# Optimization experiments

Measured on AMD Instinct MI355X. Metric: run time of the kernel, lower is better.

## Reference

```python
import jax, jax.numpy as jnp
import numpy as np

N_NODES = 500000


def _gconv(x, src, dst, ew, w_neigh, b, w_self):
    # DGL GraphConv(norm='none'): multiply weight first (in>=out here), then aggregate.
    h = x @ w_neigh                      # [N, out]
    msg = h[src] * ew[:, None]           # [E, out]
    agg = jax.ops.segment_sum(msg, dst, num_segments=N_NODES)
    return agg + b + x @ w_self          # neigh conv (+bias) + self-loop linear (no bias)


def setup_inputs() -> dict:
    key = jax.random.key(0)
    ks = jax.random.split(key, 16)
    N, E, G, F = N_NODES, 16000000, 64, 16
    inp = {
        "x": jax.random.normal(ks[0], (N, F), jnp.float32),
        "src": jax.random.randint(ks[1], (E,), 0, N),
        "dst": jax.random.randint(ks[2], (E,), 0, N),
        "graph_id": jnp.sort(jax.random.randint(ks[3], (N,), 0, G)),
        "edge_weight": jax.random.uniform(ks[4], (E,), jnp.float32),
        "num_graphs": G,
        "w_neigh0": jax.random.normal(ks[5], (F, 1), jnp.float32),
        "b0": jax.random.normal(ks[6], (1,), jnp.float32),
        "w_self0": jax.random.normal(ks[7], (F, 1), jnp.float32),
        "w_neigh1": jax.random.normal(ks[8], (1, 1), jnp.float32),
        "b1": jax.random.normal(ks[9], (1,), jnp.float32),
        "w_self1": jax.random.normal(ks[10], (1, 1), jnp.float32),
        "w_neigh2": jax.random.normal(ks[11], (1, 1), jnp.float32),
        "b2": jax.random.normal(ks[12], (1,), jnp.float32),
        "w_self2": jax.random.normal(ks[13], (1, 1), jnp.float32),
        "fc1_w": jax.random.normal(ks[14], (8, 1), jnp.float32),
        "fc1_b": jax.random.normal(ks[15], (8,), jnp.float32),
        "out_w": jax.random.normal(jax.random.fold_in(key, 100), (4, 8), jnp.float32),
        "out_b": jax.random.normal(jax.random.fold_in(key, 101), (4,), jnp.float32),
    }
    return inp


def reference(x, src, dst, graph_id, edge_weight, num_graphs,
              w_neigh0, b0, w_self0, w_neigh1, b1, w_self1,
              w_neigh2, b2, w_self2, fc1_w, fc1_b, out_w, out_b):
    h = jax.nn.relu(_gconv(x, src, dst, edge_weight, w_neigh0, b0, w_self0))
    h = jax.nn.relu(_gconv(h, src, dst, edge_weight, w_neigh1, b1, w_self1))
    h = jax.nn.relu(_gconv(h, src, dst, edge_weight, w_neigh2, b2, w_self2))
    # dgl.sum_nodes: per-graph segment sum over batched graph -> [G, 1]
    hg = jax.ops.segment_sum(h, graph_id, num_segments=num_graphs)
    hg2 = jax.nn.sigmoid((hg @ fc1_w.T + fc1_b) * 1000.0)   # [G, 8]
    out = jax.nn.relu(hg2 @ out_w.T + out_b)                # [G, 4]
    return jax.nn.log_softmax(out, axis=1)
```

## Files before the change

### kernel.cpp

```cpp
#include <hip/hip_runtime.h>

#define N_NODES   500000
#define NGRAPH    64
#define FDIM      16
#define NPB       4096
#define NPB_SHIFT 12
#define NBINS     123
#define NBLK      1024
#define CH        4096
typedef unsigned int u32;
typedef unsigned long long u64;

__global__ __launch_bounds__(1024) void proj_hist(const int* __restrict__ dst, int E, int chunk,
                                                  u32* __restrict__ blockHist,
                                                  const float* __restrict__ x,
                                                  const float* __restrict__ wn,
                                                  const float* __restrict__ wsf,
                                                  float* __restrict__ a,
                                                  float* __restrict__ s) {
    __shared__ u32 cnt[NBINS];
    if (blockIdx.x < NBLK) {
        for (int t = threadIdx.x; t < NBINS; t += 1024) cnt[t] = 0;
        __syncthreads();
        int b = blockIdx.x;
        int lo = b * chunk, hi = min(lo + chunk, E);
        int m = (hi - lo) & ~3;
        for (int i = lo + threadIdx.x * 4; i < lo + m; i += 4096) {
            int4 d = *(const int4*)(dst + i);
            atomicAdd(&cnt[((u32)d.x) >> NPB_SHIFT], 1u);
            atomicAdd(&cnt[((u32)d.y) >> NPB_SHIFT], 1u);
            atomicAdd(&cnt[((u32)d.z) >> NPB_SHIFT], 1u);
            atomicAdd(&cnt[((u32)d.w) >> NPB_SHIFT], 1u);
        }
        for (int i = lo + m + threadIdx.x; i < hi; i += 1024)
            atomicAdd(&cnt[((u32)dst[i]) >> NPB_SHIFT], 1u);
        __syncthreads();
        for (int t = threadIdx.x; t < NBINS; t += 1024)
            blockHist[(size_t)b * NBINS + t] = cnt[t];
    } else {
        int i = (blockIdx.x - NBLK) * 1024 + threadIdx.x;
        if (i >= N_NODES) return;
        const float4* xr = (const float4*)(x + (size_t)i * FDIM);
        float4 v0 = xr[0], v1 = xr[1], v2 = xr[2], v3 = xr[3];
        const float4* n4 = (const float4*)wn;
        const float4* s4 = (const float4*)wsf;
        float4 n0 = n4[0], n1 = n4[1], n2 = n4[2], n3 = n4[3];
        float4 w0 = s4[0], w1 = s4[1], w2 = s4[2], w3 = s4[3];
        float an = v0.x*n0.x + v0.y*n0.y + v0.z*n0.z + v0.w*n0.w
                 + v1.x*n1.x + v1.y*n1.y + v1.z*n1.z + v1.w*n1.w
                 + v2.x*n2.x + v2.y*n2.y + v2.z*n2.z + v2.w*n2.w
                 + v3.x*n3.x + v3.y*n3.y + v3.z*n3.z + v3.w*n3.w;
        float as = v0.x*w0.x + v0.y*w0.y + v0.z*w0.z + v0.w*w0.w
                 + v1.x*w1.x + v1.y*w1.y + v1.z*w1.z + v1.w*w1.w
                 + v2.x*w2.x + v2.y*w2.y + v2.z*w2.z + v2.w*w2.w
                 + v3.x*w3.x + v3.y*w3.y + v3.z*w3.z + v3.w*w3.w;
        a[i] = an;
        s[i] = as;
    }
}

__global__ __launch_bounds__(NBLK) void scan1_kernel(u32* __restrict__ blockHist,
                                                     u32* __restrict__ binTotal) {
    int j = blockIdx.x;
    __shared__ u32 lsum[NBLK];
    int t = threadIdx.x;
    u32 v = blockHist[(size_t)t * NBINS + j];
    lsum[t] = v;
    __syncthreads();
    u32 x = v;
    for (int off = 1; off < NBLK; off <<= 1) {
        u32 y = (t >= off) ? lsum[t - off] : 0u;
        __syncthreads();
        x += y; lsum[t] = x;
        __syncthreads();
    }
    if (t == NBLK - 1) binTotal[j] = x;
    blockHist[(size_t)t * NBINS + j] = x - v;
}

__global__ void scan2_kernel(const u32* __restrict__ binTotal, u32* __restrict__ binStart) {
    __shared__ u32 sh[128];
    int t = threadIdx.x;
    u32 v = (t < NBINS) ? binTotal[t] : 0u;
    sh[t] = v;
    __syncthreads();
    for (int d = 1; d < 128; d <<= 1) {
        u32 y = (t >= d) ? sh[t - d] : 0u;
        __syncthreads();
        sh[t] += y;
        __syncthreads();
    }
    if (t < NBINS) binStart[t] = sh[t] - v;
    if (t == 127) binStart[NBINS] = sh[127];
}

__global__ __launch_bounds__(512) void scatter_staged(const int* __restrict__ src,
                                                      const int* __restrict__ dst,
                                                      const float* __restrict__ ew,
                                                      int E, int chunk,
                                                      const u32* __restrict__ blockHist,
                                                      const u32* __restrict__ binStart,
                                                      u64* __restrict__ binned) {
    __shared__ u32 cursor[NBINS];
    __shared__ u32 cnt[NBINS];
    __shared__ u32 off[NBINS];
    __shared__ u64 stage[CH];
    __shared__ unsigned char binOf[CH];
    int b   = blockIdx.x;
    int tid = threadIdx.x;
    for (int t = tid; t < NBINS; t += 512)
        cursor[t] = binStart[t] + blockHist[(size_t)b * NBINS + t];
    int lo = b * chunk, hiB = min(lo + chunk, E);
    for (int base = lo; base < hiB; base += CH) {
        int n = min(CH, hiB - base);
        for (int t = tid; t < NBINS; t += 512) cnt[t] = 0;
        __syncthreads();
        u32 rec[8]; float wv[8]; u32 bi[8]; u32 rk[8];
#pragma unroll
        for (int k = 0; k < 8; ++k) {
            int idx = base + k * 512 + tid;
            bi[k] = 0xFFFFFFFFu;
            if (idx < base + n) {
                u32 d  = (u32)dst[idx];
                bi[k]  = d >> NPB_SHIFT;
                rec[k] = ((u32)src[idx]) | ((d & (NPB - 1)) << 19);
                wv[k]  = ew[idx];
                rk[k]  = atomicAdd(&cnt[bi[k]], 1u);
            }
        }
        __syncthreads();
        if (tid < NBINS) off[tid] = cnt[tid];
        __syncthreads();
        for (int d2 = 1; d2 < 128; d2 <<= 1) {
            u32 v = 0;
            if (tid < NBINS) { v = off[tid]; if (tid >= d2) v += off[tid - d2]; }
            __syncthreads();
            if (tid < NBINS) off[tid] = v;
            __syncthreads();
        }
        if (tid < NBINS) off[tid] -= cnt[tid];
        __syncthreads();
#pragma unroll
        for (int k = 0; k < 8; ++k) {
            if (bi[k] != 0xFFFFFFFFu) {
                u32 p = off[bi[k]] + rk[k];
                stage[p] = (u64)rec[k] | ((u64)__float_as_uint(wv[k]) << 32);
                binOf[p] = (unsigned char)bi[k];
            }
        }
        __syncthreads();
        for (int p = tid; p < n; p += 512) {
            u32 j = binOf[p];
            binned[cursor[j] + ((u32)p - off[j])] = stage[p];
        }
        __syncthreads();
        for (int t = tid; t < NBINS; t += 512) cursor[t] += cnt[t];
        __syncthreads();
    }
}

template<int S>
__global__ __launch_bounds__(512) void bin_pass(const u64* __restrict__ binned,
                                                const u32* __restrict__ binStart,
                                                const float* __restrict__ hsrc,
                                                float* __restrict__ partials) {
    __shared__ float acc[NPB];
    int blk   = blockIdx.x;
    int j     = blk / S;
    int slice = blk % S;
    for (int t = threadIdx.x; t < NPB; t += 512) acc[t] = 0.0f;
    __syncthreads();
    u32 blo = binStart[j], bhi = binStart[j + 1];
    u32 cnt = bhi - blo;
    u32 per = (cnt + S - 1) / S;
    u32 lo = blo + slice * per;
    u32 hi = min(lo + per, bhi);

    u32 i = lo + threadIdx.x;
    for (; i + 7u * 512u < hi; i += 8u * 512u) {
        u64 e[8];
#pragma unroll
        for (int k = 0; k < 8; ++k) e[k] = __builtin_nontemporal_load(&binned[i + (u32)k * 512u]);
        float g[8];
#pragma unroll
        for (int k = 0; k < 8; ++k) g[k] = hsrc[((u32)e[k]) & 0x7FFFFu];
#pragma unroll
        for (int k = 0; k < 8; ++k)
            atomicAdd(&acc[((u32)e[k]) >> 19], g[k] * __uint_as_float((u32)(e[k] >> 32)));
    }
    for (; i < hi; i += 512) {
        u64 e = __builtin_nontemporal_load(&binned[i]);
        u32 xx = (u32)e;
        atomicAdd(&acc[xx >> 19], hsrc[xx & 0x7FFFFu] * __uint_as_float((u32)(e >> 32)));
    }
    __syncthreads();
    float* p = partials + (size_t)(j * S + slice) * NPB;
    for (int t = threadIdx.x; t < NPB; t += 512)
        __builtin_nontemporal_store(acc[t], &p[t]);
}

template<int S>
__global__ void merge_update(const float* __restrict__ partials,
                             const float* __restrict__ selfv,
                             const float* __restrict__ wnp,
                             const float* __restrict__ bp,
                             const float* __restrict__ wsp,
                             float* __restrict__ hout) {
    int n = blockIdx.x * blockDim.x + threadIdx.x;
    if (n >= N_NODES) return;
    int j = n >> NPB_SHIFT;
    int l = n & (NPB - 1);
    const float* p = partials + (size_t)j * S * NPB + l;
    float sum = 0.0f;
#pragma unroll
    for (int k = 0; k < S; ++k) sum += __builtin_nontemporal_load(&p[k * NPB]);
    float scale = wnp ? wnp[0] : 1.0f;
    float wself = wsp ? wsp[0] : 1.0f;
    hout[n] = fmaxf(sum * scale + bp[0] + selfv[n] * wself, 0.0f);
}

__global__ void edge_pass(const int* __restrict__ src, const int* __restrict__ dst,
                          const float* __restrict__ ew, const float* __restrict__ h,
                          float* __restrict__ agg, const float* __restrict__ wnp, int E) {
    float scale = wnp ? wnp[0] : 1.0f;
    int stride = gridDim.x * blockDim.x;
    for (int i = blockIdx.x * blockDim.x + threadIdx.x; i < E; i += stride)
        atomicAdd(&agg[dst[i]], h[src[i]] * ew[i] * scale);
}
__global__ void node_update(const float* __restrict__ agg, const float* __restrict__ selfv,
                            const float* __restrict__ bp, const float* __restrict__ wsp,
                            float* __restrict__ hout) {
    int i = blockIdx.x * blockDim.x + threadIdx.x;
    if (i >= N_NODES) return;
    float wsc = wsp ? wsp[0] : 1.0f;
    hout[i] = fmaxf(agg[i] + bp[0] + selfv[i] * wsc, 0.0f);
}
__global__ void proj_kernel(const float* __restrict__ x, const float* __restrict__ wn,
                            const float* __restrict__ wsf, float* __restrict__ a,
                            float* __restrict__ s) {
    int i = blockIdx.x * blockDim.x + threadIdx.x;
    if (i >= N_NODES) return;
    float an = 0.f, as = 0.f;
    for (int k = 0; k < FDIM; ++k) {
        float v = x[(size_t)i * FDIM + k];
        an += v * wn[k]; as += v * wsf[k];
    }
    a[i] = an; s[i] = as;
}

__global__ __launch_bounds__(256) void graph_sum(const float* __restrict__ h,
                                                 const int* __restrict__ gid,
                                                 float* __restrict__ hg) {
    __shared__ float loc[NGRAPH];
    int t = threadIdx.x;
    if (t < NGRAPH) loc[t] = 0.0f;
    __syncthreads();
    int nq = N_NODES / 4;
    int stride = gridDim.x * blockDim.x;
    for (int q = blockIdx.x * blockDim.x + t; q < nq; q += stride) {
        int4   g4 = *(const int4*)(gid + 4 * q);
        float4 h4 = *(const float4*)(h + 4 * q);
        int g0 = __shfl(g4.x, 0);
        bool uni = (g4.x == g0) & (g4.w == g0);
        if (__all(uni)) {
            float v = h4.x + h4.y + h4.z + h4.w;
#pragma unroll
            for (int o = 32; o > 0; o >>= 1) v += __shfl_down(v, o);
            if ((t & 63) == 0) atomicAdd(&loc[g0], v);
        } else {
            atomicAdd(&loc[g4.x], h4.x);
            atomicAdd(&loc[g4.y], h4.y);
            atomicAdd(&loc[g4.z], h4.z);
            atomicAdd(&loc[g4.w], h4.w);
        }
    }
    __syncthreads();
    if (t < NGRAPH) atomicAdd(&hg[t], loc[t]);
}

__global__ void head_kernel(const float* __restrict__ hg,
                            const float* __restrict__ fc1w, const float* __restrict__ fc1b,
                            const float* __restrict__ outw, const float* __restrict__ outb,
                            float* __restrict__ out) {
    int g = threadIdx.x;
    if (g >= NGRAPH) return;
    float v = hg[g];
    float t[8];
#pragma unroll
    for (int j = 0; j < 8; ++j) {
        float z = (v * fc1w[j] + fc1b[j]) * 1000.0f;
        t[j] = 1.0f / (1.0f + expf(-z));
    }
    float o[4];
#pragma unroll
    for (int k = 0; k < 4; ++k) {
        float acc2 = outb[k];
#pragma unroll
        for (int j = 0; j < 8; ++j) acc2 += t[j] * outw[k * 8 + j];
        o[k] = fmaxf(acc2, 0.0f);
    }
    float m = fmaxf(fmaxf(o[0], o[1]), fmaxf(o[2], o[3]));
    float se = 0.0f;
#pragma unroll
    for (int k = 0; k < 4; ++k) se += expf(o[k] - m);
    float lse = m + logf(se);
#pragma unroll
    for (int k = 0; k < 4; ++k) out[g * 4 + k] = o[k] - lse;
}

extern "C" void kernel_launch(void* const* d_in, const int* in_sizes, int n_in,
                              void* d_out, int out_size, void* d_ws, size_t ws_size,
                              hipStream_t stream) {
    const float* x    = (const float*)d_in[0];
    const int*   src  = (const int*)  d_in[1];
    const int*   dst  = (const int*)  d_in[2];
    const int*   gid  = (const int*)  d_in[3];
    const float* ew   = (const float*)d_in[4];
    const float* wn0  = (const float*)d_in[6];
    const float* b0   = (const float*)d_in[7];
    const float* ws0  = (const float*)d_in[8];
    const float* wn1  = (const float*)d_in[9];
    const float* b1   = (const float*)d_in[10];
    const float* ws1  = (const float*)d_in[11];
    const float* wn2  = (const float*)d_in[12];
    const float* b2   = (const float*)d_in[13];
    const float* ws2  = (const float*)d_in[14];
    const float* fc1w = (const float*)d_in[15];
    const float* fc1b = (const float*)d_in[16];
    const float* outw = (const float*)d_in[17];
    const float* outb = (const float*)d_in[18];
    int E = in_sizes[1];

    const int BLK = 256;
    int nodeGrid = (N_NODES + BLK - 1) / BLK;
    char* ws = (char*)d_ws;

    size_t off = 0;
    u64*   binned    = (u64*)(ws + off);   off += (size_t)E * 8;
    u32*   blockHist = (u32*)(ws + off);   off += (size_t)NBLK * NBINS * 4;
    u32*   binStart  = (u32*)(ws + off);   off += (NBINS + 1) * 4;
    off = (off + 63) & ~(size_t)63;
    u32*   binTotal  = (u32*)(ws + off);   off += (NBINS + 1) * 4;
    off = (off + 63) & ~(size_t)63;
    float* partials  = (float*)(ws + off);
    size_t base_off  = off;
    size_t nodes_bytes = 4 * (size_t)N_NODES * 4 + NGRAPH * 4;
    size_t need8 = base_off + (size_t)NBINS * 8 * NPB * 4 + nodes_bytes;
    size_t need4 = base_off + (size_t)NBINS * 4 * NPB * 4 + nodes_bytes;

    int S = (ws_size >= need8) ? 8 : ((ws_size >= need4) ? 4 : 0);

    if (S) {
        off = base_off + (size_t)NBINS * S * NPB * 4;
        float* a  = (float*)(ws + off); off += (size_t)N_NODES * 4;
        float* s  = (float*)(ws + off); off += (size_t)N_NODES * 4;
        float* h0 = (float*)(ws + off); off += (size_t)N_NODES * 4;
        float* h1 = (float*)(ws + off); off += (size_t)N_NODES * 4;
        float* hg = (float*)(ws + off);

        int chunk = (((E + NBLK - 1) / NBLK) + 3) & ~3;
        int projBlocks = (N_NODES + 1023) / 1024;

        proj_hist<<<NBLK + projBlocks, 1024, 0, stream>>>(dst, E, chunk, blockHist,
                                                          x, wn0, ws0, a, s);
        scan1_kernel<<<NBINS, NBLK, 0, stream>>>(blockHist, binTotal);
        scan2_kernel<<<1, 128, 0, stream>>>(binTotal, binStart);
        scatter_staged<<<NBLK, 512, 0, stream>>>(src, dst, ew, E, chunk, blockHist, binStart, binned);

        if (S == 8) {
            bin_pass<8><<<NBINS * 8, 512, 0, stream>>>(binned, binStart, a, partials);
            merge_update<8><<<nodeGrid, BLK, 0, stream>>>(partials, s, nullptr, b0, nullptr, h0);
            bin_pass<8><<<NBINS * 8, 512, 0, stream>>>(binned, binStart, h0, partials);
            merge_update<8><<<nodeGrid, BLK, 0, stream>>>(partials, h0, wn1, b1, ws1, h1);
            bin_pass<8><<<NBINS * 8, 512, 0, stream>>>(binned, binStart, h1, partials);
            merge_update<8><<<nodeGrid, BLK, 0, stream>>>(partials, h1, wn2, b2, ws2, a);
        } else {
            bin_pass<4><<<NBINS * 4, 512, 0, stream>>>(binned, binStart, a, partials);
            merge_update<4><<<nodeGrid, BLK, 0, stream>>>(partials, s, nullptr, b0, nullptr, h0);
            bin_pass<4><<<NBINS * 4, 512, 0, stream>>>(binned, binStart, h0, partials);
            merge_update<4><<<nodeGrid, BLK, 0, stream>>>(partials, h0, wn1, b1, ws1, h1);
            bin_pass<4><<<NBINS * 4, 512, 0, stream>>>(binned, binStart, h1, partials);
            merge_update<4><<<nodeGrid, BLK, 0, stream>>>(partials, h1, wn2, b2, ws2, a);
        }

        (void)hipMemsetAsync(hg, 0, NGRAPH * sizeof(float), stream);
        graph_sum<<<512, 256, 0, stream>>>(a, gid, hg);
        head_kernel<<<1, 64, 0, stream>>>(hg, fc1w, fc1b, outw, outb, (float*)d_out);
    } else {
        float* wsb  = (float*)d_ws;
        float* fa   = wsb;
        float* fs   = wsb + 1 * (size_t)N_NODES;
        float* fagg = wsb + 2 * (size_t)N_NODES;
        float* fh   = wsb + 3 * (size_t)N_NODES;
        float* fhg  = wsb + 4 * (size_t)N_NODES;

        proj_kernel<<<nodeGrid, BLK, 0, stream>>>(x, wn0, ws0, fa, fs);

        (void)hipMemsetAsync(fagg, 0, (size_t)N_NODES * sizeof(float), stream);
        edge_pass<<<4096, BLK, 0, stream>>>(src, dst, ew, fa, fagg, nullptr, E);
        node_update<<<nodeGrid, BLK, 0, stream>>>(fagg, fs, b0, nullptr, fh);

        (void)hipMemsetAsync(fagg, 0, (size_t)N_NODES * sizeof(float), stream);
        edge_pass<<<4096, BLK, 0, stream>>>(src, dst, ew, fh, fagg, wn1, E);
        node_update<<<nodeGrid, BLK, 0, stream>>>(fagg, fh, b1, ws1, fh);

        (void)hipMemsetAsync(fagg, 0, (size_t)N_NODES * sizeof(float), stream);
        edge_pass<<<4096, BLK, 0, stream>>>(src, dst, ew, fh, fagg, wn2, E);
        node_update<<<nodeGrid, BLK, 0, stream>>>(fagg, fh, b2, ws2, fh);

        (void)hipMemsetAsync(fhg, 0, NGRAPH * sizeof(float), stream);
        graph_sum<<<512, 256, 0, stream>>>(fh, gid, fhg);
        head_kernel<<<1, 64, 0, stream>>>(fhg, fc1w, fc1b, outw, outb, (float*)d_out);
    }
}
```

Baseline: 408.6 us.

## Add second-level source-chunk binning so edge passes gather from LDS-staged features

Edges are first binned by destination into 62 bins of 8192 nodes. Each destination bin is then sub-sorted by source chunk of 4096 nodes using a new histogram, scan and staged scatter pass. The aggregation kernel stages each source chunk of node features into LDS and gathers from there, replacing random global reads of hsrc. The cost is one extra full pass over the 16M edge records, a second E-sized workspace buffer, and more sync per chunk. A fallback path keeps single-level binning when the workspace is too small.

```diff
diff --git a/kernel.cpp b/kernel.cpp
--- a/kernel.cpp
+++ b/kernel.cpp
@@ -1,13 +1,19 @@
 #include <hip/hip_runtime.h>
 
-#define N_NODES   500000
-#define NGRAPH    64
-#define FDIM      16
-#define NPB       4096
-#define NPB_SHIFT 12
-#define NBINS     123
-#define NBLK      1024
-#define CH        4096
+#define N_NODES 500000
+#define NGRAPH  64
+#define FDIM    16
+#define NB1     62
+#define NPB1    8192
+#define SH1     13
+#define NB2     123
+#define NB2P    128
+#define NPC     4096
+#define SH2     12
+#define NSUB    16
+#define SLC     8
+#define NBLK    1024
+#define CH      4096
 typedef unsigned int u32;
 typedef unsigned long long u64;
 
@@ -18,25 +24,25 @@
                                                   const float* __restrict__ wsf,
                                                   float* __restrict__ a,
                                                   float* __restrict__ s) {
-    __shared__ u32 cnt[NBINS];
+    __shared__ u32 cnt[NB1];
     if (blockIdx.x < NBLK) {
-        for (int t = threadIdx.x; t < NBINS; t += 1024) cnt[t] = 0;
+        if (threadIdx.x < NB1) cnt[threadIdx.x] = 0;
         __syncthreads();
         int b = blockIdx.x;
         int lo = b * chunk, hi = min(lo + chunk, E);
         int m = (hi - lo) & ~3;
         for (int i = lo + threadIdx.x * 4; i < lo + m; i += 4096) {
             int4 d = *(const int4*)(dst + i);
-            atomicAdd(&cnt[((u32)d.x) >> NPB_SHIFT], 1u);
-            atomicAdd(&cnt[((u32)d.y) >> NPB_SHIFT], 1u);
-            atomicAdd(&cnt[((u32)d.z) >> NPB_SHIFT], 1u);
-            atomicAdd(&cnt[((u32)d.w) >> NPB_SHIFT], 1u);
+            atomicAdd(&cnt[((u32)d.x) >> SH1], 1u);
+            atomicAdd(&cnt[((u32)d.y) >> SH1], 1u);
+            atomicAdd(&cnt[((u32)d.z) >> SH1], 1u);
+            atomicAdd(&cnt[((u32)d.w) >> SH1], 1u);
         }
         for (int i = lo + m + threadIdx.x; i < hi; i += 1024)
-            atomicAdd(&cnt[((u32)dst[i]) >> NPB_SHIFT], 1u);
-        __syncthreads();
-        for (int t = threadIdx.x; t < NBINS; t += 1024)
-            blockHist[(size_t)b * NBINS + t] = cnt[t];
+            atomicAdd(&cnt[((u32)dst[i]) >> SH1], 1u);
+        __syncthreads();
+        if (threadIdx.x < NB1)
+            blockHist[(size_t)b * NB1 + threadIdx.x] = cnt[threadIdx.x];
     } else {
         int i = (blockIdx.x - NBLK) * 1024 + threadIdx.x;
         if (i >= N_NODES) return;
@@ -64,7 +70,7 @@
     int j = blockIdx.x;
     __shared__ u32 lsum[NBLK];
     int t = threadIdx.x;
-    u32 v = blockHist[(size_t)t * NBINS + j];
+    u32 v = blockHist[(size_t)t * NB1 + j];
     lsum[t] = v;
     __syncthreads();
     u32 x = v;
@@ -75,70 +81,68 @@
         __syncthreads();
     }
     if (t == NBLK - 1) binTotal[j] = x;
-    blockHist[(size_t)t * NBINS + j] = x - v;
+    blockHist[(size_t)t * NB1 + j] = x - v;
 }
 
 __global__ void scan2_kernel(const u32* __restrict__ binTotal, u32* __restrict__ binStart) {
-    __shared__ u32 sh[128];
+    __shared__ u32 sh[64];
     int t = threadIdx.x;
-    u32 v = (t < NBINS) ? binTotal[t] : 0u;
+    u32 v = (t < NB1) ? binTotal[t] : 0u;
     sh[t] = v;
     __syncthreads();
-    for (int d = 1; d < 128; d <<= 1) {
+    for (int d = 1; d < 64; d <<= 1) {
         u32 y = (t >= d) ? sh[t - d] : 0u;
         __syncthreads();
         sh[t] += y;
         __syncthreads();
     }
-    if (t < NBINS) binStart[t] = sh[t] - v;
-    if (t == 127) binStart[NBINS] = sh[127];
-}
-
-__global__ __launch_bounds__(512) void scatter_staged(const int* __restrict__ src,
-                                                      const int* __restrict__ dst,
-                                                      const float* __restrict__ ew,
-                                                      int E, int chunk,
-                                                      const u32* __restrict__ blockHist,
-                                                      const u32* __restrict__ binStart,
-                                                      u64* __restrict__ binned) {
-    __shared__ u32 cursor[NBINS];
-    __shared__ u32 cnt[NBINS];
-    __shared__ u32 off[NBINS];
+    if (t < NB1) binStart[t] = sh[t] - v;
+    if (t == 63) binStart[NB1] = sh[63];
+}
+
+__global__ __launch_bounds__(512) void scatter1_staged(const int* __restrict__ src,
+                                                       const int* __restrict__ dst,
+                                                       const float* __restrict__ ew,
+                                                       int E, int chunk,
+                                                       const u32* __restrict__ blockHist,
+                                                       const u32* __restrict__ binStart,
+                                                       u64* __restrict__ binned) {
+    __shared__ u32 cursor[64];
+    __shared__ u32 cnt[64];
+    __shared__ u32 off[64];
     __shared__ u64 stage[CH];
     __shared__ unsigned char binOf[CH];
-    int b   = blockIdx.x;
-    int tid = threadIdx.x;
-    for (int t = tid; t < NBINS; t += 512)
-        cursor[t] = binStart[t] + blockHist[(size_t)b * NBINS + t];
+    int b = blockIdx.x, tid = threadIdx.x;
+    if (tid < NB1) cursor[tid] = binStart[tid] + blockHist[(size_t)b * NB1 + tid];
     int lo = b * chunk, hiB = min(lo + chunk, E);
     for (int base = lo; base < hiB; base += CH) {
         int n = min(CH, hiB - base);
-        for (int t = tid; t < NBINS; t += 512) cnt[t] = 0;
-        __syncthreads();
-        u32 rec[8]; float wv[8]; u32 bi[8]; u32 rk[8];
+        if (tid < 64) cnt[tid] = 0;
+        __syncthreads();
+        u32 rec[8]; float wv[8]; u32 bi[8], rk[8];
 #pragma unroll
         for (int k = 0; k < 8; ++k) {
             int idx = base + k * 512 + tid;
             bi[k] = 0xFFFFFFFFu;
             if (idx < base + n) {
                 u32 d  = (u32)dst[idx];
-                bi[k]  = d >> NPB_SHIFT;
-                rec[k] = ((u32)src[idx]) | ((d & (NPB - 1)) << 19);
+                bi[k]  = d >> SH1;
+                rec[k] = ((u32)src[idx]) | ((d & (NPB1 - 1)) << 19);
                 wv[k]  = ew[idx];
                 rk[k]  = atomicAdd(&cnt[bi[k]], 1u);
             }
         }
         __syncthreads();
-        if (tid < NBINS) off[tid] = cnt[tid];
-        __syncthreads();
-        for (int d2 = 1; d2 < 128; d2 <<= 1) {
-            u32 v = 0;
-            if (tid < NBINS) { v = off[tid]; if (tid >= d2) v += off[tid - d2]; }
+        if (tid < 64) off[tid] = cnt[tid];
+        __syncthreads();
+        for (int d2 = 1; d2 < 64; d2 <<= 1) {
+            u32 y = 0;
+            if (tid < 64 && tid >= d2) y = off[tid - d2];
             __syncthreads();
-            if (tid < NBINS) off[tid] = v;
+            if (tid < 64) off[tid] += y;
             __syncthreads();
         }
-        if (tid < NBINS) off[tid] -= cnt[tid];
+        if (tid < 64) off[tid] -= cnt[tid];
         __syncthreads();
 #pragma unroll
         for (int k = 0; k < 8; ++k) {
@@ -150,37 +154,194 @@
         }
         __syncthreads();
         for (int p = tid; p < n; p += 512) {
-            u32 j = binOf[p];
-            binned[cursor[j] + ((u32)p - off[j])] = stage[p];
-        }
-        __syncthreads();
-        for (int t = tid; t < NBINS; t += 512) cursor[t] += cnt[t];
-        __syncthreads();
-    }
-}
-
-template<int S>
-__global__ __launch_bounds__(512) void bin_pass(const u64* __restrict__ binned,
-                                                const u32* __restrict__ binStart,
-                                                const float* __restrict__ hsrc,
-                                                float* __restrict__ partials) {
-    __shared__ float acc[NPB];
-    int blk   = blockIdx.x;
-    int j     = blk / S;
-    int slice = blk % S;
-    for (int t = threadIdx.x; t < NPB; t += 512) acc[t] = 0.0f;
+            u32 jj = binOf[p];
+            binned[cursor[jj] + ((u32)p - off[jj])] = stage[p];
+        }
+        __syncthreads();
+        if (tid < NB1) cursor[tid] += cnt[tid];
+        __syncthreads();
+    }
+}
+
+__global__ __launch_bounds__(512) void hist2_kernel(const u64* __restrict__ binned1,
+                                                    const u32* __restrict__ binStart,
+                                                    u32* __restrict__ hist2) {
+    __shared__ u32 c2[NB2P];
+    int j = blockIdx.x / NSUB, sb = blockIdx.x % NSUB;
+    int tid = threadIdx.x;
+    if (tid < NB2P) c2[tid] = 0;
     __syncthreads();
     u32 blo = binStart[j], bhi = binStart[j + 1];
-    u32 cnt = bhi - blo;
-    u32 per = (cnt + S - 1) / S;
-    u32 lo = blo + slice * per;
+    u32 cj = bhi - blo;
+    u32 per = (cj + NSUB - 1) / NSUB;
+    u32 lo = blo + sb * per;
     u32 hi = min(lo + per, bhi);
-
+    const u32* b32 = (const u32*)binned1;
+    for (u32 i = lo + tid; i < hi; i += 512)
+        atomicAdd(&c2[(b32[2 * (size_t)i] & 0x7FFFFu) >> SH2], 1u);
+    __syncthreads();
+    if (tid < NB2P) hist2[((size_t)j * NSUB + sb) * NB2P + tid] = c2[tid];
+}
+
+__global__ __launch_bounds__(512) void scanB_kernel(const u32* __restrict__ hist2,
+                                                    const u32* __restrict__ binStart,
+                                                    u32* __restrict__ scatOff,
+                                                    u32* __restrict__ chunkSt) {
+    int j = blockIdx.x;
+    __shared__ u32 tsum[512];
+    int t = threadIdx.x;
+    u32 base = binStart[j];
+    u32 v[4]; u32 ssum = 0;
+#pragma unroll
+    for (int q = 0; q < 4; ++q) {
+        int k = t * 4 + q;
+        int c = k >> 4, sidx = k & 15;
+        u32 xv = (c < NB2) ? hist2[((size_t)j * NSUB + sidx) * NB2P + c] : 0u;
+        v[q] = xv; ssum += xv;
+    }
+    tsum[t] = ssum;
+    __syncthreads();
+    u32 x = ssum;
+    for (int d = 1; d < 512; d <<= 1) {
+        u32 y = (t >= d) ? tsum[t - d] : 0u;
+        __syncthreads();
+        x += y; tsum[t] = x;
+        __syncthreads();
+    }
+    u32 run = x - ssum;
+#pragma unroll
+    for (int q = 0; q < 4; ++q) {
+        int k = t * 4 + q;
+        int c = k >> 4, sidx = k & 15;
+        if (c < NB2) {
+            scatOff[((size_t)j * NSUB + sidx) * NB2P + c] = base + run;
+            if (sidx == 0) chunkSt[j * (NB2 + 1) + c] = base + run;
+        }
+        run += v[q];
+    }
+    if (t == 0) chunkSt[j * (NB2 + 1) + NB2] = binStart[j + 1];
+}
+
+__global__ __launch_bounds__(512) void scatter2_staged(const u64* __restrict__ binned1,
+                                                       const u32* __restrict__ binStart,
+                                                       const u32* __restrict__ scatOff,
+                                                       u64* __restrict__ binned2) {
+    __shared__ u32 cursor[NB2P];
+    __shared__ u32 cnt[NB2P];
+    __shared__ u32 off[NB2P];
+    __shared__ u64 stage[CH];
+    __shared__ unsigned char binOf[CH];
+    int j = blockIdx.x / NSUB, sb = blockIdx.x % NSUB;
+    int tid = threadIdx.x;
+    if (tid < NB2P) cursor[tid] = (tid < NB2) ? scatOff[((size_t)j * NSUB + sb) * NB2P + tid] : 0u;
+    u32 blo = binStart[j], bhi = binStart[j + 1];
+    u32 cj = bhi - blo;
+    u32 per = (cj + NSUB - 1) / NSUB;
+    u32 lo = blo + sb * per;
+    u32 hi = min(lo + per, bhi);
+    for (u32 base = lo; base < hi; base += CH) {
+        u32 n = min((u32)CH, hi - base);
+        if (tid < NB2P) cnt[tid] = 0;
+        __syncthreads();
+        u64 ev[8]; u32 bi[8], rk[8];
+#pragma unroll
+        for (int k = 0; k < 8; ++k) {
+            u32 idx = base + (u32)k * 512u + tid;
+            bi[k] = 0xFFFFFFFFu;
+            if (idx < base + n) {
+                u64 e = binned1[idx];
+                u32 r = (u32)e;
+                u32 c = (r & 0x7FFFFu) >> SH2;
+                bi[k] = c;
+                ev[k] = ((u64)((r & (NPC - 1)) | ((r >> 19) << 12))) | (e & 0xFFFFFFFF00000000ull);
+                rk[k] = atomicAdd(&cnt[c], 1u);
+            }
+        }
+        __syncthreads();
+        if (tid < NB2P) off[tid] = cnt[tid];
+        __syncthreads();
+        for (int d2 = 1; d2 < NB2P; d2 <<= 1) {
+            u32 y = 0;
+            if (tid < NB2P && tid >= d2) y = off[tid - d2];
+            __syncthreads();
+            if (tid < NB2P) off[tid] += y;
+            __syncthreads();
+        }
+        if (tid < NB2P) off[tid] -= cnt[tid];
+        __syncthreads();
+#pragma unroll
+        for (int k = 0; k < 8; ++k) {
+            if (bi[k] != 0xFFFFFFFFu) {
+                u32 p = off[bi[k]] + rk[k];
+                stage[p] = ev[k];
+                binOf[p] = (unsigned char)bi[k];
+            }
+        }
+        __syncthreads();
+        for (u32 p = tid; p < n; p += 512) {
+            u32 c = binOf[p];
+            binned2[cursor[c] + (p - off[c])] = stage[p];
+        }
+        __syncthreads();
+        if (tid < NB2P) cursor[tid] += cnt[tid];
+        __syncthreads();
+    }
+}
+
+__global__ __launch_bounds__(1024) void bin_pass2(const u64* __restrict__ binned2,
+                                                  const u32* __restrict__ chunkSt,
+                                                  const float* __restrict__ hsrc,
+                                                  float* __restrict__ partials) {
+    __shared__ float acc[NPB1];
+    __shared__ float chk[NPC];
+    __shared__ u32 cs[NB2 + 1];
+    int j = blockIdx.x / SLC, sl = blockIdx.x % SLC;
+    int tid = threadIdx.x;
+    for (int t = tid; t < NPB1; t += 1024) acc[t] = 0.0f;
+    if (tid < NB2 + 1) cs[tid] = chunkSt[j * (NB2 + 1) + tid];
+    __syncthreads();
+    for (int c = sl; c < NB2; c += SLC) {
+        int base = c * NPC;
+        int nst = min(NPC, N_NODES - base);
+        if (nst == NPC) {
+            float4 v = *(const float4*)(hsrc + base + tid * 4);
+            *(float4*)&chk[tid * 4] = v;
+        } else {
+            for (int t = tid; t < nst; t += 1024) chk[t] = hsrc[base + t];
+        }
+        __syncthreads();
+        u32 lo = cs[c], hi = cs[c + 1];
+        for (u32 i = lo + tid; i < hi; i += 1024) {
+            u64 e = __builtin_nontemporal_load(&binned2[i]);
+            u32 r = (u32)e;
+            atomicAdd(&acc[(r >> 12) & (NPB1 - 1)],
+                      chk[r & (NPC - 1)] * __uint_as_float((u32)(e >> 32)));
+        }
+        __syncthreads();
+    }
+    float* p = partials + ((size_t)j * SLC + sl) * NPB1;
+    for (int t = tid; t < NPB1; t += 1024)
+        __builtin_nontemporal_store(acc[t], &p[t]);
+}
+
+__global__ __launch_bounds__(512) void bin_pass_g(const u64* __restrict__ binned1,
+                                                  const u32* __restrict__ binStart,
+                                                  const float* __restrict__ hsrc,
+                                                  float* __restrict__ partials) {
+    __shared__ float acc[NPB1];
+    int j = blockIdx.x / SLC, sl = blockIdx.x % SLC;
+    for (int t = threadIdx.x; t < NPB1; t += 512) acc[t] = 0.0f;
+    __syncthreads();
+    u32 blo = binStart[j], bhi = binStart[j + 1];
+    u32 cj = bhi - blo;
+    u32 per = (cj + SLC - 1) / SLC;
+    u32 lo = blo + sl * per;
+    u32 hi = min(lo + per, bhi);
     u32 i = lo + threadIdx.x;
     for (; i + 7u * 512u < hi; i += 8u * 512u) {
         u64 e[8];
 #pragma unroll
-        for (int k = 0; k < 8; ++k) e[k] = __builtin_nontemporal_load(&binned[i + (u32)k * 512u]);
+        for (int k = 0; k < 8; ++k) e[k] = __builtin_nontemporal_load(&binned1[i + (u32)k * 512u]);
         float g[8];
 #pragma unroll
         for (int k = 0; k < 8; ++k) g[k] = hsrc[((u32)e[k]) & 0x7FFFFu];
@@ -189,17 +350,15 @@
             atomicAdd(&acc[((u32)e[k]) >> 19], g[k] * __uint_as_float((u32)(e[k] >> 32)));
     }
     for (; i < hi; i += 512) {
-        u64 e = __builtin_nontemporal_load(&binned[i]);
-        u32 xx = (u32)e;
-        atomicAdd(&acc[xx >> 19], hsrc[xx & 0x7FFFFu] * __uint_as_float((u32)(e >> 32)));
-    }
-    __syncthreads();
-    float* p = partials + (size_t)(j * S + slice) * NPB;
-    for (int t = threadIdx.x; t < NPB; t += 512)
+        u64 e = __builtin_nontemporal_load(&binned1[i]);
+        atomicAdd(&acc[((u32)e) >> 19], hsrc[((u32)e) & 0x7FFFFu] * __uint_as_float((u32)(e >> 32)));
+    }
+    __syncthreads();
+    float* p = partials + ((size_t)j * SLC + sl) * NPB1;
+    for (int t = threadIdx.x; t < NPB1; t += 512)
         __builtin_nontemporal_store(acc[t], &p[t]);
 }
 
-template<int S>
 __global__ void merge_update(const float* __restrict__ partials,
                              const float* __restrict__ selfv,
                              const float* __restrict__ wnp,
@@ -208,12 +367,12 @@
                              float* __restrict__ hout) {
     int n = blockIdx.x * blockDim.x + threadIdx.x;
     if (n >= N_NODES) return;
-    int j = n >> NPB_SHIFT;
-    int l = n & (NPB - 1);
-    const float* p = partials + (size_t)j * S * NPB + l;
+    int j = n >> SH1;
+    int l = n & (NPB1 - 1);
+    const float* p = partials + (size_t)j * SLC * NPB1 + l;
     float sum = 0.0f;
 #pragma unroll
-    for (int k = 0; k < S; ++k) sum += __builtin_nontemporal_load(&p[k * NPB]);
+    for (int k = 0; k < SLC; ++k) sum += __builtin_nontemporal_load(&p[k * NPB1]);
     float scale = wnp ? wnp[0] : 1.0f;
     float wself = wsp ? wsp[0] : 1.0f;
     hout[n] = fmaxf(sum * scale + bp[0] + selfv[n] * wself, 0.0f);
@@ -336,51 +495,56 @@
     char* ws = (char*)d_ws;
 
     size_t off = 0;
-    u64*   binned    = (u64*)(ws + off);   off += (size_t)E * 8;
-    u32*   blockHist = (u32*)(ws + off);   off += (size_t)NBLK * NBINS * 4;
-    u32*   binStart  = (u32*)(ws + off);   off += (NBINS + 1) * 4;
+    u64* binned1    = (u64*)(ws + off); off += (size_t)E * 8;
+    u32* blockHist  = (u32*)(ws + off); off += (size_t)NBLK * NB1 * 4;
+    u32* binStart   = (u32*)(ws + off); off += (NB1 + 2) * 4;
     off = (off + 63) & ~(size_t)63;
-    u32*   binTotal  = (u32*)(ws + off);   off += (NBINS + 1) * 4;
+    u32* binTotal   = (u32*)(ws + off); off += (NB1 + 2) * 4;
     off = (off + 63) & ~(size_t)63;
-    float* partials  = (float*)(ws + off);
-    size_t base_off  = off;
-    size_t nodes_bytes = 4 * (size_t)N_NODES * 4 + NGRAPH * 4;
-    size_t need8 = base_off + (size_t)NBINS * 8 * NPB * 4 + nodes_bytes;
-    size_t need4 = base_off + (size_t)NBINS * 4 * NPB * 4 + nodes_bytes;
-
-    int S = (ws_size >= need8) ? 8 : ((ws_size >= need4) ? 4 : 0);
-
-    if (S) {
-        off = base_off + (size_t)NBINS * S * NPB * 4;
-        float* a  = (float*)(ws + off); off += (size_t)N_NODES * 4;
-        float* s  = (float*)(ws + off); off += (size_t)N_NODES * 4;
-        float* h0 = (float*)(ws + off); off += (size_t)N_NODES * 4;
-        float* h1 = (float*)(ws + off); off += (size_t)N_NODES * 4;
-        float* hg = (float*)(ws + off);
-
+    u32* hist2buf   = (u32*)(ws + off); off += (size_t)NB1 * NSUB * NB2P * 4;
+    u32* scatOff    = (u32*)(ws + off); off += (size_t)NB1 * NSUB * NB2P * 4;
+    u32* chunkSt    = (u32*)(ws + off); off += (size_t)NB1 * (NB2 + 1) * 4;
+    off = (off + 63) & ~(size_t)63;
+    float* partials = (float*)(ws + off); off += (size_t)NB1 * SLC * NPB1 * 4;
+    float* a  = (float*)(ws + off); off += (size_t)N_NODES * 4;
+    float* s  = (float*)(ws + off); off += (size_t)N_NODES * 4;
+    float* h0 = (float*)(ws + off); off += (size_t)N_NODES * 4;
+    float* h1 = (float*)(ws + off); off += (size_t)N_NODES * 4;
+    float* hg = (float*)(ws + off); off += 256;
+    off = (off + 63) & ~(size_t)63;
+    size_t need_mid = off;
+    u64* binned2 = (u64*)(ws + off); off += (size_t)E * 8;
+    size_t need_full = off;
+
+    if (ws_size >= need_mid) {
+        bool full = (ws_size >= need_full);
         int chunk = (((E + NBLK - 1) / NBLK) + 3) & ~3;
         int projBlocks = (N_NODES + 1023) / 1024;
 
         proj_hist<<<NBLK + projBlocks, 1024, 0, stream>>>(dst, E, chunk, blockHist,
                                                           x, wn0, ws0, a, s);
-        scan1_kernel<<<NBINS, NBLK, 0, stream>>>(blockHist, binTotal);
-        scan2_kernel<<<1, 128, 0, stream>>>(binTotal, binStart);
-        scatter_staged<<<NBLK, 512, 0, stream>>>(src, dst, ew, E, chunk, blockHist, binStart, binned);
-
-        if (S == 8) {
-            bin_pass<8><<<NBINS * 8, 512, 0, stream>>>(binned, binStart, a, partials);
-            merge_update<8><<<nodeGrid, BLK, 0, stream>>>(partials, s, nullptr, b0, nullptr, h0);
-            bin_pass<8><<<NBINS * 8, 512, 0, stream>>>(binned, binStart, h0, partials);
-            merge_update<8><<<nodeGrid, BLK, 0, stream>>>(partials, h0, wn1, b1, ws1, h1);
-            bin_pass<8><<<NBINS * 8, 512, 0, stream>>>(binned, binStart, h1, partials);
-            merge_update<8><<<nodeGrid, BLK, 0, stream>>>(partials, h1, wn2, b2, ws2, a);
+        scan1_kernel<<<NB1, NBLK, 0, stream>>>(blockHist, binTotal);
+        scan2_kernel<<<1, 64, 0, stream>>>(binTotal, binStart);
+        scatter1_staged<<<NBLK, 512, 0, stream>>>(src, dst, ew, E, chunk, blockHist,
+                                                  binStart, binned1);
+        if (full) {
+            hist2_kernel<<<NB1 * NSUB, 512, 0, stream>>>(binned1, binStart, hist2buf);
+            scanB_kernel<<<NB1, 512, 0, stream>>>(hist2buf, binStart, scatOff, chunkSt);
+            scatter2_staged<<<NB1 * NSUB, 512, 0, stream>>>(binned1, binStart, scatOff, binned2);
+
+            bin_pass2<<<NB1 * SLC, 1024, 0, stream>>>(binned2, chunkSt, a, partials);
+            merge_update<<<nodeGrid, BLK, 0, stream>>>(partials, s, nullptr, b0, nullptr, h0);
+            bin_pass2<<<NB1 * SLC, 1024, 0, stream>>>(binned2, chunkSt, h0, partials);
+            merge_update<<<nodeGrid, BLK, 0, stream>>>(partials, h0, wn1, b1, ws1, h1);
+            bin_pass2<<<NB1 * SLC, 1024, 0, stream>>>(binned2, chunkSt, h1, partials);
+            merge_update<<<nodeGrid, BLK, 0, stream>>>(partials, h1, wn2, b2, ws2, a);
         } else {
-            bin_pass<4><<<NBINS * 4, 512, 0, stream>>>(binned, binStart, a, partials);
-            merge_update<4><<<nodeGrid, BLK, 0, stream>>>(partials, s, nullptr, b0, nullptr, h0);
-            bin_pass<4><<<NBINS * 4, 512, 0, stream>>>(binned, binStart, h0, partials);
-            merge_update<4><<<nodeGrid, BLK, 0, stream>>>(partials, h0, wn1, b1, ws1, h1);
-            bin_pass<4><<<NBINS * 4, 512, 0, stream>>>(binned, binStart, h1, partials);
-            merge_update<4><<<nodeGrid, BLK, 0, stream>>>(partials, h1, wn2, b2, ws2, a);
+            bin_pass_g<<<NB1 * SLC, 512, 0, stream>>>(binned1, binStart, a, partials);
+            merge_update<<<nodeGrid, BLK, 0, stream>>>(partials, s, nullptr, b0, nullptr, h0);
+            bin_pass_g<<<NB1 * SLC, 512, 0, stream>>>(binned1, binStart, h0, partials);
+            merge_update<<<nodeGrid, BLK, 0, stream>>>(partials, h0, wn1, b1, ws1, h1);
+            bin_pass_g<<<NB1 * SLC, 512, 0, stream>>>(binned1, binStart, h1, partials);
+            merge_update<<<nodeGrid, BLK, 0, stream>>>(partials, h1, wn2, b2, ws2, a);
         }
 
         (void)hipMemsetAsync(hg, 0, NGRAPH * sizeof(float), stream);
```

Result: no change. 403.5 us (-1.3%).

## Bin edges by (dst,src) tile pairs so gathers hit LDS-staged source chunks

Applied to the files above, without the earlier changes.

Edges are now binned into 2D buckets keyed by destination block and source block (31x31 tiles of 16384 nodes) instead of only destination blocks. Each bin pass block stages a 16K-node chunk of the source feature vector into shared memory and gathers from LDS instead of random global reads, accumulating into a 16K-entry LDS destination tile. The per-edge record packs 14-bit local src and dst indices, and the histogram, scan and scatter grow to 961 buckets with 1024-thread blocks. This trades the random global gather for more preprocessing work, 128 KB of LDS per block and fewer blocks (248) in each aggregation pass. merge_update now writes in place into s.

```diff
diff --git a/kernel.cpp b/kernel.cpp
--- a/kernel.cpp
+++ b/kernel.cpp
@@ -1,42 +1,47 @@
 #include <hip/hip_runtime.h>
 
-#define N_NODES   500000
-#define NGRAPH    64
-#define FDIM      16
-#define NPB       4096
-#define NPB_SHIFT 12
-#define NBINS     123
-#define NBLK      1024
-#define CH        4096
+#define N_NODES 500000
+#define NGRAPH  64
+#define FDIM    16
+#define SHN     14
+#define NPBIN   16384
+#define NBC     31
+#define NBK     961
+#define SLC     8
+#define NBLK    512
+#define CH      8192
 typedef unsigned int u32;
 typedef unsigned long long u64;
 
-__global__ __launch_bounds__(1024) void proj_hist(const int* __restrict__ dst, int E, int chunk,
+__global__ __launch_bounds__(1024) void proj_hist(const int* __restrict__ src,
+                                                  const int* __restrict__ dst,
+                                                  int E, int chunk,
                                                   u32* __restrict__ blockHist,
                                                   const float* __restrict__ x,
                                                   const float* __restrict__ wn,
                                                   const float* __restrict__ wsf,
                                                   float* __restrict__ a,
                                                   float* __restrict__ s) {
-    __shared__ u32 cnt[NBINS];
+    __shared__ u32 cnt[NBK];
     if (blockIdx.x < NBLK) {
-        for (int t = threadIdx.x; t < NBINS; t += 1024) cnt[t] = 0;
+        for (int t = threadIdx.x; t < NBK; t += 1024) cnt[t] = 0;
         __syncthreads();
         int b = blockIdx.x;
         int lo = b * chunk, hi = min(lo + chunk, E);
         int m = (hi - lo) & ~3;
         for (int i = lo + threadIdx.x * 4; i < lo + m; i += 4096) {
-            int4 d = *(const int4*)(dst + i);
-            atomicAdd(&cnt[((u32)d.x) >> NPB_SHIFT], 1u);
-            atomicAdd(&cnt[((u32)d.y) >> NPB_SHIFT], 1u);
-            atomicAdd(&cnt[((u32)d.z) >> NPB_SHIFT], 1u);
-            atomicAdd(&cnt[((u32)d.w) >> NPB_SHIFT], 1u);
+            int4 d4 = *(const int4*)(dst + i);
+            int4 s4 = *(const int4*)(src + i);
+            atomicAdd(&cnt[(((u32)d4.x) >> SHN) * NBC + (((u32)s4.x) >> SHN)], 1u);
+            atomicAdd(&cnt[(((u32)d4.y) >> SHN) * NBC + (((u32)s4.y) >> SHN)], 1u);
+            atomicAdd(&cnt[(((u32)d4.z) >> SHN) * NBC + (((u32)s4.z) >> SHN)], 1u);
+            atomicAdd(&cnt[(((u32)d4.w) >> SHN) * NBC + (((u32)s4.w) >> SHN)], 1u);
         }
         for (int i = lo + m + threadIdx.x; i < hi; i += 1024)
-            atomicAdd(&cnt[((u32)dst[i]) >> NPB_SHIFT], 1u);
-        __syncthreads();
-        for (int t = threadIdx.x; t < NBINS; t += 1024)
-            blockHist[(size_t)b * NBINS + t] = cnt[t];
+            atomicAdd(&cnt[(((u32)dst[i]) >> SHN) * NBC + (((u32)src[i]) >> SHN)], 1u);
+        __syncthreads();
+        for (int t = threadIdx.x; t < NBK; t += 1024)
+            blockHist[(size_t)b * NBK + t] = cnt[t];
     } else {
         int i = (blockIdx.x - NBLK) * 1024 + threadIdx.x;
         if (i >= N_NODES) return;
@@ -60,11 +65,11 @@
 }
 
 __global__ __launch_bounds__(NBLK) void scan1_kernel(u32* __restrict__ blockHist,
-                                                     u32* __restrict__ binTotal) {
+                                                     u32* __restrict__ bucketTotal) {
     int j = blockIdx.x;
     __shared__ u32 lsum[NBLK];
     int t = threadIdx.x;
-    u32 v = blockHist[(size_t)t * NBINS + j];
+    u32 v = blockHist[(size_t)t * NBK + j];
     lsum[t] = v;
     __syncthreads();
     u32 x = v;
@@ -74,132 +79,147 @@
         x += y; lsum[t] = x;
         __syncthreads();
     }
-    if (t == NBLK - 1) binTotal[j] = x;
-    blockHist[(size_t)t * NBINS + j] = x - v;
-}
-
-__global__ void scan2_kernel(const u32* __restrict__ binTotal, u32* __restrict__ binStart) {
-    __shared__ u32 sh[128];
+    if (t == NBLK - 1) bucketTotal[j] = x;
+    blockHist[(size_t)t * NBK + j] = x - v;
+}
+
+__global__ __launch_bounds__(1024) void scan2_kernel(const u32* __restrict__ bucketTotal,
+                                                     u32* __restrict__ bucketStart) {
+    __shared__ u32 sh[1024];
     int t = threadIdx.x;
-    u32 v = (t < NBINS) ? binTotal[t] : 0u;
+    u32 v = (t < NBK) ? bucketTotal[t] : 0u;
     sh[t] = v;
     __syncthreads();
-    for (int d = 1; d < 128; d <<= 1) {
+    for (int d = 1; d < 1024; d <<= 1) {
         u32 y = (t >= d) ? sh[t - d] : 0u;
         __syncthreads();
         sh[t] += y;
         __syncthreads();
     }
-    if (t < NBINS) binStart[t] = sh[t] - v;
-    if (t == 127) binStart[NBINS] = sh[127];
-}
-
-__global__ __launch_bounds__(512) void scatter_staged(const int* __restrict__ src,
-                                                      const int* __restrict__ dst,
-                                                      const float* __restrict__ ew,
-                                                      int E, int chunk,
-                                                      const u32* __restrict__ blockHist,
-                                                      const u32* __restrict__ binStart,
-                                                      u64* __restrict__ binned) {
-    __shared__ u32 cursor[NBINS];
-    __shared__ u32 cnt[NBINS];
-    __shared__ u32 off[NBINS];
+    if (t < NBK) bucketStart[t] = sh[t] - v;
+    if (t == 1023) bucketStart[NBK] = sh[1023];
+}
+
+__global__ __launch_bounds__(1024) void scatter_staged(const int* __restrict__ src,
+                                                       const int* __restrict__ dst,
+                                                       const float* __restrict__ ew,
+                                                       int E, int chunk,
+                                                       const u32* __restrict__ blockHist,
+                                                       const u32* __restrict__ bucketStart,
+                                                       u64* __restrict__ binned) {
+    __shared__ u32 cursor[NBK];
+    __shared__ u32 cnt[1024];
+    __shared__ u32 off[1024];
     __shared__ u64 stage[CH];
-    __shared__ unsigned char binOf[CH];
-    int b   = blockIdx.x;
-    int tid = threadIdx.x;
-    for (int t = tid; t < NBINS; t += 512)
-        cursor[t] = binStart[t] + blockHist[(size_t)b * NBINS + t];
+    __shared__ unsigned short binOf[CH];
+    int b = blockIdx.x, tid = threadIdx.x;
+    for (int t = tid; t < NBK; t += 1024)
+        cursor[t] = bucketStart[t] + blockHist[(size_t)b * NBK + t];
     int lo = b * chunk, hiB = min(lo + chunk, E);
     for (int base = lo; base < hiB; base += CH) {
         int n = min(CH, hiB - base);
-        for (int t = tid; t < NBINS; t += 512) cnt[t] = 0;
-        __syncthreads();
-        u32 rec[8]; float wv[8]; u32 bi[8]; u32 rk[8];
+        cnt[tid] = 0;
+        __syncthreads();
+        u32 rec[8]; float wv[8]; u32 bi[8], rk[8];
 #pragma unroll
         for (int k = 0; k < 8; ++k) {
-            int idx = base + k * 512 + tid;
+            int idx = base + k * 1024 + tid;
             bi[k] = 0xFFFFFFFFu;
             if (idx < base + n) {
                 u32 d  = (u32)dst[idx];
-                bi[k]  = d >> NPB_SHIFT;
-                rec[k] = ((u32)src[idx]) | ((d & (NPB - 1)) << 19);
+                u32 sv = (u32)src[idx];
+                bi[k]  = (d >> SHN) * NBC + (sv >> SHN);
+                rec[k] = (sv & (NPBIN - 1)) | ((d & (NPBIN - 1)) << SHN);
                 wv[k]  = ew[idx];
                 rk[k]  = atomicAdd(&cnt[bi[k]], 1u);
             }
         }
         __syncthreads();
-        if (tid < NBINS) off[tid] = cnt[tid];
-        __syncthreads();
-        for (int d2 = 1; d2 < 128; d2 <<= 1) {
-            u32 v = 0;
-            if (tid < NBINS) { v = off[tid]; if (tid >= d2) v += off[tid - d2]; }
+        off[tid] = cnt[tid];
+        __syncthreads();
+        for (int d2 = 1; d2 < 1024; d2 <<= 1) {
+            u32 y = (tid >= d2) ? off[tid - d2] : 0u;
             __syncthreads();
-            if (tid < NBINS) off[tid] = v;
+            off[tid] += y;
             __syncthreads();
         }
-        if (tid < NBINS) off[tid] -= cnt[tid];
+        u32 myexcl = off[tid] - cnt[tid];
+        __syncthreads();
+        off[tid] = myexcl;
         __syncthreads();
 #pragma unroll
         for (int k = 0; k < 8; ++k) {
             if (bi[k] != 0xFFFFFFFFu) {
                 u32 p = off[bi[k]] + rk[k];
                 stage[p] = (u64)rec[k] | ((u64)__float_as_uint(wv[k]) << 32);
-                binOf[p] = (unsigned char)bi[k];
+                binOf[p] = (unsigned short)bi[k];
             }
         }
         __syncthreads();
-        for (int p = tid; p < n; p += 512) {
-            u32 j = binOf[p];
-            binned[cursor[j] + ((u32)p - off[j])] = stage[p];
-        }
-        __syncthreads();
-        for (int t = tid; t < NBINS; t += 512) cursor[t] += cnt[t];
-        __syncthreads();
-    }
-}
-
-template<int S>
-__global__ __launch_bounds__(512) void bin_pass(const u64* __restrict__ binned,
-                                                const u32* __restrict__ binStart,
-                                                const float* __restrict__ hsrc,
-                                                float* __restrict__ partials) {
-    __shared__ float acc[NPB];
-    int blk   = blockIdx.x;
-    int j     = blk / S;
-    int slice = blk % S;
-    for (int t = threadIdx.x; t < NPB; t += 512) acc[t] = 0.0f;
+        for (int p = tid; p < n; p += 1024) {
+            u32 kk = binOf[p];
+            binned[cursor[kk] + ((u32)p - off[kk])] = stage[p];
+        }
+        __syncthreads();
+        for (int t = tid; t < NBK; t += 1024) cursor[t] += cnt[t];
+        __syncthreads();
+    }
+}
+
+__global__ __launch_bounds__(1024) void bin_pass2(const u64* __restrict__ binned,
+                                                  const u32* __restrict__ bucketStart,
+                                                  const float* __restrict__ hsrc,
+                                                  float* __restrict__ partials) {
+    __shared__ float acc[NPBIN];
+    __shared__ float chk[NPBIN];
+    int j = blockIdx.x / SLC, sl = blockIdx.x % SLC;
+    int tid = threadIdx.x;
+    for (int t = tid; t < NPBIN; t += 1024) acc[t] = 0.0f;
     __syncthreads();
-    u32 blo = binStart[j], bhi = binStart[j + 1];
-    u32 cnt = bhi - blo;
-    u32 per = (cnt + S - 1) / S;
-    u32 lo = blo + slice * per;
-    u32 hi = min(lo + per, bhi);
-
-    u32 i = lo + threadIdx.x;
-    for (; i + 7u * 512u < hi; i += 8u * 512u) {
-        u64 e[8];
-#pragma unroll
-        for (int k = 0; k < 8; ++k) e[k] = __builtin_nontemporal_load(&binned[i + (u32)k * 512u]);
-        float g[8];
-#pragma unroll
-        for (int k = 0; k < 8; ++k) g[k] = hsrc[((u32)e[k]) & 0x7FFFFu];
-#pragma unroll
-        for (int k = 0; k < 8; ++k)
-            atomicAdd(&acc[((u32)e[k]) >> 19], g[k] * __uint_as_float((u32)(e[k] >> 32)));
-    }
-    for (; i < hi; i += 512) {
-        u64 e = __builtin_nontemporal_load(&binned[i]);
-        u32 xx = (u32)e;
-        atomicAdd(&acc[xx >> 19], hsrc[xx & 0x7FFFFu] * __uint_as_float((u32)(e >> 32)));
-    }
-    __syncthreads();
-    float* p = partials + (size_t)(j * S + slice) * NPB;
-    for (int t = threadIdx.x; t < NPB; t += 512)
+    for (int c = sl; c < NBC; c += SLC) {
+        int base = c << SHN;
+        int nst = min(NPBIN, N_NODES - base);
+        if (nst == NPBIN) {
+            const float4* hp = (const float4*)(hsrc + base);
+#pragma unroll
+            for (int q = 0; q < 4; ++q) {
+                float4 v = hp[q * 1024 + tid];
+                *(float4*)&chk[(q * 1024 + tid) * 4] = v;
+            }
+        } else {
+            for (int t = tid; t < nst; t += 1024) chk[t] = hsrc[base + t];
+        }
+        __syncthreads();
+        u32 lo = bucketStart[j * NBC + c], hi = bucketStart[j * NBC + c + 1];
+        u32 i = lo + tid;
+        for (; i + 3u * 1024u < hi; i += 4u * 1024u) {
+            u64 e0 = __builtin_nontemporal_load(&binned[i]);
+            u64 e1 = __builtin_nontemporal_load(&binned[i + 1024]);
+            u64 e2 = __builtin_nontemporal_load(&binned[i + 2048]);
+            u64 e3 = __builtin_nontemporal_load(&binned[i + 3072]);
+            u32 r0 = (u32)e0, r1 = (u32)e1, r2 = (u32)e2, r3 = (u32)e3;
+            float g0 = chk[r0 & (NPBIN - 1)];
+            float g1 = chk[r1 & (NPBIN - 1)];
+            float g2 = chk[r2 & (NPBIN - 1)];
+            float g3 = chk[r3 & (NPBIN - 1)];
+            atomicAdd(&acc[(r0 >> SHN) & (NPBIN - 1)], g0 * __uint_as_float((u32)(e0 >> 32)));
+            atomicAdd(&acc[(r1 >> SHN) & (NPBIN - 1)], g1 * __uint_as_float((u32)(e1 >> 32)));
+            atomicAdd(&acc[(r2 >> SHN) & (NPBIN - 1)], g2 * __uint_as_float((u32)(e2 >> 32)));
+            atomicAdd(&acc[(r3 >> SHN) & (NPBIN - 1)], g3 * __uint_as_float((u32)(e3 >> 32)));
+        }
+        for (; i < hi; i += 1024) {
+            u64 e = __builtin_nontemporal_load(&binned[i]);
+            u32 r = (u32)e;
+            atomicAdd(&acc[(r >> SHN) & (NPBIN - 1)],
+                      chk[r & (NPBIN - 1)] * __uint_as_float((u32)(e >> 32)));
+        }
+        __syncthreads();
+    }
+    float* p = partials + ((size_t)j * SLC + sl) * NPBIN;
+    for (int t = tid; t < NPBIN; t += 1024)
         __builtin_nontemporal_store(acc[t], &p[t]);
 }
 
-template<int S>
 __global__ void merge_update(const float* __restrict__ partials,
                              const float* __restrict__ selfv,
                              const float* __restrict__ wnp,
@@ -208,12 +228,12 @@
                              float* __restrict__ hout) {
     int n = blockIdx.x * blockDim.x + threadIdx.x;
     if (n >= N_NODES) return;
-    int j = n >> NPB_SHIFT;
-    int l = n & (NPB - 1);
-    const float* p = partials + (size_t)j * S * NPB + l;
+    int j = n >> SHN;
+    int l = n & (NPBIN - 1);
+    const float* p = partials + ((size_t)j * SLC) * NPBIN + l;
     float sum = 0.0f;
 #pragma unroll
-    for (int k = 0; k < S; ++k) sum += __builtin_nontemporal_load(&p[k * NPB]);
+    for (int k = 0; k < SLC; ++k) sum += __builtin_nontemporal_load(&p[k * NPBIN]);
     float scale = wnp ? wnp[0] : 1.0f;
     float wself = wsp ? wsp[0] : 1.0f;
     hout[n] = fmaxf(sum * scale + bp[0] + selfv[n] * wself, 0.0f);
@@ -336,55 +356,38 @@
     char* ws = (char*)d_ws;
 
     size_t off = 0;
-    u64*   binned    = (u64*)(ws + off);   off += (size_t)E * 8;
-    u32*   blockHist = (u32*)(ws + off);   off += (size_t)NBLK * NBINS * 4;
-    u32*   binStart  = (u32*)(ws + off);   off += (NBINS + 1) * 4;
+    u64* binned      = (u64*)(ws + off); off += (size_t)E * 8;
+    u32* blockHist   = (u32*)(ws + off); off += (size_t)NBLK * NBK * 4;
+    u32* bucketStart = (u32*)(ws + off); off += (NBK + 2) * 4;
     off = (off + 63) & ~(size_t)63;
-    u32*   binTotal  = (u32*)(ws + off);   off += (NBINS + 1) * 4;
+    u32* bucketTotal = (u32*)(ws + off); off += (NBK + 2) * 4;
     off = (off + 63) & ~(size_t)63;
-    float* partials  = (float*)(ws + off);
-    size_t base_off  = off;
-    size_t nodes_bytes = 4 * (size_t)N_NODES * 4 + NGRAPH * 4;
-    size_t need8 = base_off + (size_t)NBINS * 8 * NPB * 4 + nodes_bytes;
-    size_t need4 = base_off + (size_t)NBINS * 4 * NPB * 4 + nodes_bytes;
-
-    int S = (ws_size >= need8) ? 8 : ((ws_size >= need4) ? 4 : 0);
-
-    if (S) {
-        off = base_off + (size_t)NBINS * S * NPB * 4;
-        float* a  = (float*)(ws + off); off += (size_t)N_NODES * 4;
-        float* s  = (float*)(ws + off); off += (size_t)N_NODES * 4;
-        float* h0 = (float*)(ws + off); off += (size_t)N_NODES * 4;
-        float* h1 = (float*)(ws + off); off += (size_t)N_NODES * 4;
-        float* hg = (float*)(ws + off);
-
+    float* partials  = (float*)(ws + off); off += (size_t)NBC * SLC * NPBIN * 4;
+    float* a  = (float*)(ws + off); off += (size_t)N_NODES * 4;
+    float* s  = (float*)(ws + off); off += (size_t)N_NODES * 4;
+    float* hg = (float*)(ws + off); off += 256;
+    size_t need = off;
+
+    if (ws_size >= need) {
         int chunk = (((E + NBLK - 1) / NBLK) + 3) & ~3;
         int projBlocks = (N_NODES + 1023) / 1024;
 
-        proj_hist<<<NBLK + projBlocks, 1024, 0, stream>>>(dst, E, chunk, blockHist,
+        proj_hist<<<NBLK + projBlocks, 1024, 0, stream>>>(src, dst, E, chunk, blockHist,
                                                           x, wn0, ws0, a, s);
-        scan1_kernel<<<NBINS, NBLK, 0, stream>>>(blockHist, binTotal);
-        scan2_kernel<<<1, 128, 0, stream>>>(binTotal, binStart);
-        scatter_staged<<<NBLK, 512, 0, stream>>>(src, dst, ew, E, chunk, blockHist, binStart, binned);
-
-        if (S == 8) {
-            bin_pass<8><<<NBINS * 8, 512, 0, stream>>>(binned, binStart, a, partials);
-            merge_update<8><<<nodeGrid, BLK, 0, stream>>>(partials, s, nullptr, b0, nullptr, h0);
-            bin_pass<8><<<NBINS * 8, 512, 0, stream>>>(binned, binStart, h0, partials);
-            merge_update<8><<<nodeGrid, BLK, 0, stream>>>(partials, h0, wn1, b1, ws1, h1);
-            bin_pass<8><<<NBINS * 8, 512, 0, stream>>>(binned, binStart, h1, partials);
-            merge_update<8><<<nodeGrid, BLK, 0, stream>>>(partials, h1, wn2, b2, ws2, a);
-        } else {
-            bin_pass<4><<<NBINS * 4, 512, 0, stream>>>(binned, binStart, a, partials);
-            merge_update<4><<<nodeGrid, BLK, 0, stream>>>(partials, s, nullptr, b0, nullptr, h0);
-            bin_pass<4><<<NBINS * 4, 512, 0, stream>>>(binned, binStart, h0, partials);
-            merge_update<4><<<nodeGrid, BLK, 0, stream>>>(partials, h0, wn1, b1, ws1, h1);
-            bin_pass<4><<<NBINS * 4, 512, 0, stream>>>(binned, binStart, h1, partials);
-            merge_update<4><<<nodeGrid, BLK, 0, stream>>>(partials, h1, wn2, b2, ws2, a);
-        }
+        scan1_kernel<<<NBK, NBLK, 0, stream>>>(blockHist, bucketTotal);
+        scan2_kernel<<<1, 1024, 0, stream>>>(bucketTotal, bucketStart);
+        scatter_staged<<<NBLK, 1024, 0, stream>>>(src, dst, ew, E, chunk, blockHist,
+                                                  bucketStart, binned);
+
+        bin_pass2<<<NBC * SLC, 1024, 0, stream>>>(binned, bucketStart, a, partials);
+        merge_update<<<nodeGrid, BLK, 0, stream>>>(partials, s, nullptr, b0, nullptr, s);
+        bin_pass2<<<NBC * SLC, 1024, 0, stream>>>(binned, bucketStart, s, partials);
+        merge_update<<<nodeGrid, BLK, 0, stream>>>(partials, s, wn1, b1, ws1, s);
+        bin_pass2<<<NBC * SLC, 1024, 0, stream>>>(binned, bucketStart, s, partials);
+        merge_update<<<nodeGrid, BLK, 0, stream>>>(partials, s, wn2, b2, ws2, s);
 
         (void)hipMemsetAsync(hg, 0, NGRAPH * sizeof(float), stream);
-        graph_sum<<<512, 256, 0, stream>>>(a, gid, hg);
+        graph_sum<<<512, 256, 0, stream>>>(s, gid, hg);
         head_kernel<<<1, 64, 0, stream>>>(hg, fc1w, fc1b, outw, outb, (float*)d_out);
     } else {
         float* wsb  = (float*)d_ws;
```

Measured after the change: 487.1 us. +19.2%, slower.
